# Optimization experiments

Hardware: AMD Instinct MI355X
Metric: run time of the kernel (lower is better)

Reference implementation:

```python
import jax, jax.numpy as jnp
import numpy as np

D_MODEL = 1024
N_HEADS = 16
HEAD_DIM = D_MODEL // N_HEADS
B, L, E = 2, 2048, 256


def _linear_params(key, d_out, d_in):
    kw, kb = jax.random.split(key)
    lim = 1.0 / np.sqrt(d_in)
    W = jax.random.uniform(kw, (d_out, d_in), jnp.float32, -lim, lim)
    b = jax.random.uniform(kb, (d_out,), jnp.float32, -lim, lim)
    return W, b


def setup_inputs() -> dict:
    key = jax.random.key(0)
    ks = jax.random.split(key, 10)
    x = jax.random.normal(ks[0], (B, L, D_MODEL), jnp.float32)
    kg_embeds = jax.random.normal(ks[1], (B, E, D_MODEL), jnp.float32)
    Wq, bq = _linear_params(ks[2], D_MODEL, D_MODEL)
    Wk, bk = _linear_params(ks[3], D_MODEL, D_MODEL)
    Wv, bv = _linear_params(ks[4], D_MODEL, D_MODEL)
    Wo, bo = _linear_params(ks[5], D_MODEL, D_MODEL)
    Wkk, bkk = _linear_params(ks[6], D_MODEL, D_MODEL)
    Wkv, bkv = _linear_params(ks[7], D_MODEL, D_MODEL)
    Wg, bg = _linear_params(ks[8], D_MODEL, 2 * D_MODEL)
    return {"x": x, "kg_embeds": kg_embeds,
            "Wq": Wq, "bq": bq, "Wk": Wk, "bk": bk, "Wv": Wv, "bv": bv,
            "Wkk": Wkk, "bkk": bkk, "Wkv": Wkv, "bkv": bkv,
            "Wo": Wo, "bo": bo, "Wg": Wg, "bg": bg}


def _heads(t):
    # [B, S, D] -> [B, H, S, hd]
    Bb, S, _ = t.shape
    return t.reshape(Bb, S, N_HEADS, HEAD_DIM).transpose(0, 2, 1, 3)


def reference(x, kg_embeds, Wq, bq, Wk, bk, Wv, bv, Wkk, bkk, Wkv, bkv, Wo, bo, Wg, bg):
    scale = HEAD_DIM ** -0.5
    q = _heads(x @ Wq.T + bq)                      # [B,H,L,hd]
    k = _heads(x @ Wk.T + bk)
    v = _heads(x @ Wv.T + bv)
    k_kg = _heads(kg_embeds @ Wkk.T + bkk)         # [B,H,E,hd]
    v_kg = _heads(kg_embeds @ Wkv.T + bkv)
    k_aug = jnp.concatenate([k, k_kg], axis=2)     # [B,H,L+E,hd]
    v_aug = jnp.concatenate([v, v_kg], axis=2)
    scores = jnp.einsum('bhld,bhmd->bhlm', q, k_aug) * scale  # [B,H,L,L+E]
    attn = jax.nn.softmax(scores, axis=-1)
    out = jnp.einsum('bhlm,bhmd->bhld', attn, v_aug)           # [B,H,L,hd]
    out = out.transpose(0, 2, 1, 3).reshape(x.shape)            # [B,L,D]
    kg_global = jnp.broadcast_to(kg_embeds.mean(axis=1, keepdims=True), x.shape)
    gate = jax.nn.sigmoid(jnp.concatenate([out, kg_global], axis=-1) @ Wg.T + bg)
    return gate * (out @ Wo.T + bo) + (1.0 - gate) * x
```

## Files before the change

### kernel.cpp

```cpp
#include <hip/hip_runtime.h>
#include <stdint.h>

typedef unsigned short ushort_t;
typedef __attribute__((ext_vector_type(8))) short short8;
typedef __attribute__((ext_vector_type(4))) short short4v;
typedef __attribute__((ext_vector_type(4))) float f32x4;
typedef __attribute__((ext_vector_type(4))) unsigned uintx4;

#define DEV static __device__ __forceinline__

DEV unsigned short f2bf(float f) {
  unsigned u = __builtin_bit_cast(unsigned, f);
  u += 0x7fffu + ((u >> 16) & 1u);
  return (unsigned short)(u >> 16);
}
DEV float bf2f(unsigned short b) {
  return __builtin_bit_cast(float, (unsigned)b << 16);
}

DEV void gl16(const void* g, void* l) {
  __builtin_amdgcn_global_load_lds(
      (__attribute__((address_space(1))) char*)(unsigned long long)g,
      (__attribute__((address_space(3))) char*)(unsigned)(unsigned long long)l,
      16, 0, 0);
}

DEV f32x4 mfma_bf16(short8 a, short8 b, f32x4 c) {
  return __builtin_amdgcn_mfma_f32_16x16x32_bf16(a, b, c, 0, 0, 0);
}

DEV unsigned cvtpk(float lo, float hi) {
  unsigned r;
  asm("v_cvt_pk_bf16_f32 %0, %1, %2" : "=v"(r) : "v"(lo), "v"(hi));
  return r;
}
DEV void swap_net(unsigned& a, unsigned& b) {
  asm("v_permlane32_swap_b32 %0, %1" : "+v"(a), "+v"(b));
  asm("v_permlane16_swap_b32 %0, %1" : "+v"(a), "+v"(b));
}
DEV float redmax4(float x) {
  unsigned a = __builtin_bit_cast(unsigned, x), b = a;
  asm("v_permlane16_swap_b32 %0, %1" : "+v"(a), "+v"(b));
  float y = fmaxf(__builtin_bit_cast(float, a), __builtin_bit_cast(float, b));
  unsigned c = __builtin_bit_cast(unsigned, y), d = c;
  asm("v_permlane32_swap_b32 %0, %1" : "+v"(c), "+v"(d));
  return fmaxf(__builtin_bit_cast(float, c), __builtin_bit_cast(float, d));
}
DEV float lanebcast(float v, int srclane) {
  return __builtin_bit_cast(float,
      __builtin_amdgcn_ds_bpermute(srclane * 4, __builtin_bit_cast(int, v)));
}

__global__ __launch_bounds__(256) void k_cvt_all(
    const float* __restrict__ x, const float* __restrict__ kg,
    const float* __restrict__ Wq, const float* __restrict__ Wk, const float* __restrict__ Wv,
    const float* __restrict__ Wkk, const float* __restrict__ Wkv,
    const float* __restrict__ Wo, const float* __restrict__ Wg,
    ushort_t* __restrict__ xh, ushort_t* __restrict__ kgh,
    ushort_t* __restrict__ WB1, ushort_t* __restrict__ WB2, ushort_t* __restrict__ WB3) {
  const int b = blockIdx.x;
  if (b >= 10752) {
    const int i = (b - 10752) * 256 + threadIdx.x;
    const int r = i >> 8, c = (i & 255) * 4;
    const float4 v = *(const float4*)(Wg + (size_t)r * 2048 + c);
    short4v o;
    o.x = (short)f2bf(v.x); o.y = (short)f2bf(v.y); o.z = (short)f2bf(v.z); o.w = (short)f2bf(v.w);
    *(short4v*)(WB3 + 1048576 + (size_t)r * 1024 + c) = o;
    return;
  }
  const float* src;
  ushort_t* dst;
  int off;
  if (b < 4096)       { src = x;   dst = xh;            off = b; }
  else if (b < 4608)  { src = kg;  dst = kgh;           off = b - 4096; }
  else if (b < 5632)  { src = Wq;  dst = WB1;           off = b - 4608; }
  else if (b < 6656)  { src = Wk;  dst = WB1 + 1048576; off = b - 5632; }
  else if (b < 7680)  { src = Wv;  dst = WB1 + 2097152; off = b - 6656; }
  else if (b < 8704)  { src = Wkk; dst = WB2;           off = b - 7680; }
  else if (b < 9728)  { src = Wkv; dst = WB2 + 1048576; off = b - 8704; }
  else                { src = Wo;  dst = WB3;           off = b - 9728; }
  const int i = off * 1024 + threadIdx.x * 4;
  const float4 v = *(const float4*)(src + i);
  short4v o;
  o.x = (short)f2bf(v.x); o.y = (short)f2bf(v.y); o.z = (short)f2bf(v.z); o.w = (short)f2bf(v.w);
  *(short4v*)(dst + i) = o;
}

__global__ __launch_bounds__(256) void k_kgmean(const float* __restrict__ kg, float* __restrict__ out) {
  const int i = blockIdx.x * 256 + threadIdx.x;
  const int b = i >> 10, d = i & 1023;
  float s = 0.f;
  #pragma unroll 4
  for (int e = 0; e < 256; e++) s += kg[((size_t)b * 256 + e) * 1024 + d];
  out[i] = s * (1.0f / 256.0f);
}

__global__ __launch_bounds__(256) void k_g2(const float* __restrict__ kgm, const float* __restrict__ Wg,
                                            const float* __restrict__ bg, float* __restrict__ g2) {
  const int w = threadIdx.x >> 6, l = threadIdx.x & 63;
  const int idx = blockIdx.x * 4 + w;
  const int b = idx >> 10, n = idx & 1023;
  const float* wr = Wg + (size_t)n * 2048 + 1024;
  const float* mb = kgm + b * 1024;
  float s = 0.f;
  #pragma unroll
  for (int j = 0; j < 16; j++) s += mb[j * 64 + l] * wr[j * 64 + l];
  #pragma unroll
  for (int m = 32; m >= 1; m >>= 1) s += __shfl_xor(s, m);
  if (l == 0) g2[idx] = s + bg[n];
}

__global__ __launch_bounds__(256, 3) void k_mm128(
    const ushort_t* __restrict__ A0, const ushort_t* __restrict__ B0,
    const ushort_t* __restrict__ A1, const ushort_t* __restrict__ B1,
    const float* __restrict__ f0, const float* __restrict__ f1, const float* __restrict__ f2,
    const float* __restrict__ f3, const float* __restrict__ f4,
    ushort_t* __restrict__ o0, ushort_t* __restrict__ o1, ushort_t* __restrict__ o2) {
  __shared__ __align__(16) char SHb[49152];
  const int tid = threadIdx.x;
  const int w = tid >> 6, l = tid & 63;
  const int wr = w >> 1, wc = w & 1;
  const int fr = l & 15, fg = l >> 4;

  int m0, n0, iskg = 0;
  {
    const int wg = ((int)blockIdx.x & 7) * 104 + ((int)blockIdx.x >> 3);
    if (wg < 768) { m0 = (wg / 24) * 128; n0 = (wg % 24) * 128; }
    else          { const int k = wg - 768; iskg = 1; m0 = (k >> 4) * 128; n0 = (k & 15) * 128; }
  }
  const ushort_t* A = iskg ? A1 : A0;
  const ushort_t* B = iskg ? B1 : B0;

  int grow[2], gcb[2];
  #pragma unroll
  for (int j = 0; j < 2; j++) {
    const int beta = j * 256 + tid;
    const int rp = beta >> 3;
    const int u = (beta & 7) ^ (rp & 7);
    grow[j] = 2 * rp + (u >> 2);
    gcb[j] = u & 3;
  }
  const char* gA[2];
  const char* gB[2];
  #pragma unroll
  for (int j = 0; j < 2; j++) {
    gA[j] = (const char*)A + (size_t)(m0 + grow[j]) * 2048 + gcb[j] * 16;
    gB[j] = (const char*)B + (size_t)(n0 + grow[j]) * 2048 + gcb[j] * 16;
  }

  auto stage = [&](int s, int kt) {
    char* As = SHb + s * 16384;
    char* Bs = As + 8192;
    const int ko = kt * 64;
    #pragma unroll
    for (int j = 0; j < 2; j++) {
      gl16(gA[j] + ko, As + j * 4096 + tid * 16);
      gl16(gB[j] + ko, Bs + j * 4096 + tid * 16);
    }
  };

  int aoff[4], boff[4];
  #pragma unroll
  for (int i = 0; i < 4; i++) {
    const int rowa = wr * 64 + i * 16 + fr;
    aoff[i] = (rowa >> 1) * 128 + ((((rowa & 1) << 6) | (fg << 4)) ^ (((rowa >> 1) & 7) << 4));
    const int rowb = wc * 64 + i * 16 + fr;
    boff[i] = (rowb >> 1) * 128 + ((((rowb & 1) << 6) | (fg << 4)) ^ (((rowb >> 1) & 7) << 4));
  }

  f32x4 acc[4][4] = {};

  stage(0, 0);
  stage(1, 1);
  int sc = 0, sn2 = 2;
  for (int kt = 0; kt < 32; kt++) {
    if (kt < 31) asm volatile("s_waitcnt vmcnt(4)" ::: "memory");
    else         asm volatile("s_waitcnt vmcnt(0)" ::: "memory");
    __builtin_amdgcn_s_barrier();
    asm volatile("" ::: "memory");
    if (kt < 30) stage(sn2, kt + 2);
    const char* Ab = SHb + sc * 16384;
    const char* Bb = Ab + 8192;
    short8 af[4], bf[4];
    #pragma unroll
    for (int j = 0; j < 4; j++) bf[j] = *(const short8*)(Bb + boff[j]);
    #pragma unroll
    for (int i = 0; i < 4; i++) af[i] = *(const short8*)(Ab + aoff[i]);
    __builtin_amdgcn_s_setprio(1);
    #pragma unroll
    for (int i = 0; i < 4; i++)
      #pragma unroll
      for (int j = 0; j < 4; j++)
        acc[i][j] = mfma_bf16(af[i], bf[j], acc[i][j]);
    __builtin_amdgcn_s_setprio(0);
    sc++; if (sc == 3) sc = 0;
    sn2++; if (sn2 == 3) sn2 = 0;
  }
  __syncthreads();

  const int sec = n0 >> 10;
  const bool isV = (!iskg && sec == 2) || (iskg && sec == 1);

  if (isV) {
    ushort_t* SHs = (ushort_t*)SHb;
    const float* bV = iskg ? f4 : f2;
    const int bidx = iskg ? (m0 >> 8) : (m0 >> 11);
    const int colbase = iskg ? (2048 + (m0 & 255)) : (m0 & 2047);
    #pragma unroll
    for (int i = 0; i < 4; i++) {
      #pragma unroll
      for (int j = 0; j < 4; j++) {
        const int nl = wc * 64 + j * 16 + fr;
        const int ml0 = wr * 64 + i * 16 + fg * 4;
        const float bb = bV[(n0 & 1023) + nl];
        short4v pk;
        #pragma unroll
        for (int r = 0; r < 4; r++) pk[r] = (short)f2bf(acc[i][j][r] + bb);
        *(short4v*)(SHs + nl * 128 + (ml0 ^ ((nl & 7) << 3))) = pk;
      }
    }
    __syncthreads();
    const int row = tid >> 1, half = tid & 1;
    const int h = ((n0 & 1023) >> 6) + (row >> 6);
    const int d = row & 63;
    ushort_t* dst = o2 + ((size_t)(bidx * 16 + h) * 64 + d) * 2304 + colbase + half * 64;
    const ushort_t* srow2 = SHs + row * 128;
    #pragma unroll
    for (int k2 = 0; k2 < 8; k2++) {
      const int me = (half * 64 + k2 * 8) ^ ((row & 7) << 3);
      *(short8*)(dst + k2 * 8) = *(const short8*)(srow2 + me);
    }
    return;
  }

  #pragma unroll
  for (int i = 0; i < 4; i++) {
    #pragma unroll
    for (int j = 0; j < 4; j++) {
      const int nn = (n0 & 1023) + wc * 64 + j * 16 + fr;
      const int h = nn >> 6, d = nn & 63;
      #pragma unroll
      for (int r = 0; r < 4; r++) {
        const int m = m0 + wr * 64 + i * 16 + fg * 4 + r;
        const float v = acc[i][j][r];
        if (iskg) {
          const int b = m >> 8, e = m & 255;
          o1[((size_t)(b * 16 + h) * 2304 + 2048 + e) * 64 + d] = f2bf(v + f3[nn]);
        } else if (sec == 0) {
          const int b = m >> 11, lq = m & 2047;
          o0[((size_t)(b * 16 + h) * 2048 + lq) * 64 + d] = f2bf((v + f0[nn]) * 0.18033688f);
        } else {
          const int b = m >> 11, lq = m & 2047;
          o1[((size_t)(b * 16 + h) * 2304 + lq) * 64 + d] = f2bf(v + f1[nn]);
        }
      }
    }
  }
}

__global__ __launch_bounds__(256, 2) void k_mmout(
    const ushort_t* __restrict__ Og, const ushort_t* __restrict__ WB3,
    const float* __restrict__ bo, const float* __restrict__ g2v,
    const float* __restrict__ x, float* __restrict__ y) {
  __shared__ __align__(16) char SHb[61440];
  const int tid = threadIdx.x;
  const int w = tid >> 6, l = tid & 63;
  const int wr = w >> 1, wc = w & 1;
  const int fr = l & 15, fg = l >> 4;

  const int wg = ((int)blockIdx.x & 7) * 64 + ((int)blockIdx.x >> 3);
  const int m0 = (wg >> 3) * 64, n0 = (wg & 7) * 128;

  const int rpA = tid >> 3, uA = (tid & 7) ^ (rpA & 7);
  const char* gAp = (const char*)Og + (size_t)(m0 + 2 * rpA + (uA >> 2)) * 2048 + (uA & 3) * 16;
  int grow[2], gcb[2];
  #pragma unroll
  for (int j = 0; j < 2; j++) {
    const int beta = j * 256 + tid;
    const int rp = beta >> 3;
    const int u = (beta & 7) ^ (rp & 7);
    grow[j] = 2 * rp + (u >> 2);
    gcb[j] = u & 3;
  }
  const char* gBo[2];
  const char* gBg[2];
  #pragma unroll
  for (int j = 0; j < 2; j++) {
    gBo[j] = (const char*)WB3 + (size_t)(n0 + grow[j]) * 2048 + gcb[j] * 16;
    gBg[j] = (const char*)(WB3 + 1048576) + (size_t)(n0 + grow[j]) * 2048 + gcb[j] * 16;
  }

  auto stage = [&](int s, int kt) {
    char* As = SHb + s * 20480;
    const int ko = kt * 64;
    gl16(gAp + ko, As + tid * 16);
    #pragma unroll
    for (int j = 0; j < 2; j++) {
      gl16(gBo[j] + ko, As + 4096 + j * 4096 + tid * 16);
      gl16(gBg[j] + ko, As + 12288 + j * 4096 + tid * 16);
    }
  };

  int aoff[2], boff[4];
  #pragma unroll
  for (int i = 0; i < 2; i++) {
    const int rowa = wr * 32 + i * 16 + fr;
    aoff[i] = (rowa >> 1) * 128 + ((((rowa & 1) << 6) | (fg << 4)) ^ (((rowa >> 1) & 7) << 4));
  }
  #pragma unroll
  for (int j = 0; j < 4; j++) {
    const int rowb = wc * 64 + j * 16 + fr;
    boff[j] = (rowb >> 1) * 128 + ((((rowb & 1) << 6) | (fg << 4)) ^ (((rowb >> 1) & 7) << 4));
  }

  f32x4 ao[2][4] = {};
  f32x4 ag[2][4] = {};

  stage(0, 0);
  stage(1, 1);
  int sc = 0, sn2 = 2;
  for (int kt = 0; kt < 32; kt++) {
    if (kt < 31) asm volatile("s_waitcnt vmcnt(5)" ::: "memory");
    else         asm volatile("s_waitcnt vmcnt(0)" ::: "memory");
    __builtin_amdgcn_s_barrier();
    asm volatile("" ::: "memory");
    if (kt < 30) stage(sn2, kt + 2);
    const char* Ab = SHb + sc * 20480;
    short8 af[2], bof[4], bgf[4];
    #pragma unroll
    for (int i = 0; i < 2; i++) af[i] = *(const short8*)(Ab + aoff[i]);
    #pragma unroll
    for (int j = 0; j < 4; j++) {
      bof[j] = *(const short8*)(Ab + 4096 + boff[j]);
      bgf[j] = *(const short8*)(Ab + 12288 + boff[j]);
    }
    __builtin_amdgcn_s_setprio(1);
    #pragma unroll
    for (int i = 0; i < 2; i++)
      #pragma unroll
      for (int j = 0; j < 4; j++) {
        ao[i][j] = mfma_bf16(af[i], bof[j], ao[i][j]);
        ag[i][j] = mfma_bf16(af[i], bgf[j], ag[i][j]);
      }
    __builtin_amdgcn_s_setprio(0);
    sc++; if (sc == 3) sc = 0;
    sn2++; if (sn2 == 3) sn2 = 0;
  }

  const int bidx = m0 >> 11;
  #pragma unroll
  for (int i = 0; i < 2; i++) {
    #pragma unroll
    for (int j = 0; j < 4; j++) {
      const int nn = n0 + wc * 64 + j * 16 + fr;
      const float bb = bo[nn];
      const float gg = g2v[bidx * 1024 + nn];
      #pragma unroll
      for (int r = 0; r < 4; r++) {
        const int m = m0 + wr * 32 + i * 16 + fg * 4 + r;
        const float co = ao[i][j][r] + bb;
        const float cg = ag[i][j][r] + gg;
        const float gate = 1.0f / (1.0f + __builtin_amdgcn_exp2f(cg * -1.4426950408889634f));
        const float xv = x[(size_t)m * 1024 + nn];
        y[(size_t)m * 1024 + nn] = xv + gate * (co - xv);
      }
    }
  }
}

__global__ __launch_bounds__(256, 4) void k_attn(
    const ushort_t* __restrict__ Qg, const ushort_t* __restrict__ Kg,
    const ushort_t* __restrict__ Vtg, ushort_t* __restrict__ Og) {
  __shared__ __align__(16) ushort_t Ks[2][64 * 64];
  __shared__ __align__(16) ushort_t Vs[2][64 * 64];
  const int tid = threadIdx.x;
  const int w = tid >> 6, l = tid & 63;
  const int fr = l & 15, fg = l >> 4;

  const int id = blockIdx.y * gridDim.x + blockIdx.x;
  const int bh = (id & 7) * 4 + ((id >> 3) >> 5);
  const int q0 = ((id >> 3) & 31) * 64 + w * 16;

  short8 qf[2];
  {
    const short* qrow = (const short*)(Qg + ((size_t)bh * 2048 + q0 + fr) * 64);
    qf[0] = *(const short8*)(qrow + fg * 8);
    qf[1] = *(const short8*)(qrow + 32 + fg * 8);
  }

  constexpr short ONE = 0x3F80;
  const short8 ones = {ONE, ONE, ONE, ONE, ONE, ONE, ONE, ONE};

  f32x4 o[4] = {};
  f32x4 lacc = {};
  float mrun = -1.0e30f;

  const int rsub = tid >> 3;
  const int cS = ((tid & 7) * 16) ^ ((rsub & 7) << 4);
  const char* kbase = (const char*)(Kg + (size_t)bh * 2304 * 64);
  const char* vbase = (const char*)(Vtg + (size_t)bh * 64 * 2304);

  auto stage = [&](int nb, int tile) {
    #pragma unroll
    for (int j = 0; j < 2; j++) {
      const int row = j * 32 + rsub;
      gl16(kbase + (size_t)(tile * 64 + row) * 128 + cS,
           (char*)&Ks[nb][0] + j * 4096 + tid * 16);
      gl16(vbase + (size_t)row * 4608 + tile * 128 + cS,
           (char*)&Vs[nb][0] + j * 4096 + tid * 16);
    }
  };

  stage(0, 0);

  const int rswz = (fr & 7) << 4;

  for (int mt = 0; mt < 36; mt++) {
    __syncthreads();
    if (mt < 35) stage((mt + 1) & 1, mt + 1);

    const char* Kb = (const char*)&Ks[mt & 1][0];
    const char* Vb = (const char*)&Vs[mt & 1][0];

    f32x4 s[4];
    #pragma unroll
    for (int t = 0; t < 4; t++) {
      const int rb = (t * 16 + fr) * 128 + fg * 16;
      const short8 k0 = *(const short8*)(Kb + (rb ^ rswz));
      const short8 k1 = *(const short8*)(Kb + ((rb + 64) ^ rswz));
      f32x4 z = {};
      z = mfma_bf16(k0, qf[0], z);
      z = mfma_bf16(k1, qf[1], z);
      s[t] = z;
    }

    float m = fmaxf(s[0][0], s[0][1]);
    m = fmaxf(fmaxf(m, s[0][2]), s[0][3]);
    m = fmaxf(fmaxf(m, s[1][0]), s[1][1]);
    m = fmaxf(fmaxf(m, s[1][2]), s[1][3]);
    m = fmaxf(fmaxf(m, s[2][0]), s[2][1]);
    m = fmaxf(fmaxf(m, s[2][2]), s[2][3]);
    m = fmaxf(fmaxf(m, s[3][0]), s[3][1]);
    m = fmaxf(fmaxf(m, s[3][2]), s[3][3]);
    const float mx = redmax4(m);
    if (__any(mx - mrun > 11.5416f)) {
      const float mn = fmaxf(mrun, mx);
      const float al = __builtin_amdgcn_exp2f(mrun - mn);
      mrun = mn;
      float ab[4];
      #pragma unroll
      for (int r = 0; r < 4; r++) ab[r] = lanebcast(al, fg * 4 + r);
      #pragma unroll
      for (int r = 0; r < 4; r++) {
        lacc[r] *= ab[r];
        #pragma unroll
        for (int dt = 0; dt < 4; dt++) o[dt][r] *= ab[r];
      }
    }
    #pragma unroll
    for (int t = 0; t < 4; t++)
      #pragma unroll
      for (int r = 0; r < 4; r++)
        s[t][r] = __builtin_amdgcn_exp2f(s[t][r] - mrun);

    #pragma unroll
    for (int c = 0; c < 2; c++) {
      unsigned a0 = cvtpk(s[2 * c][0], s[2 * c][1]);
      unsigned b0 = cvtpk(s[2 * c + 1][0], s[2 * c + 1][1]);
      unsigned a1 = cvtpk(s[2 * c][2], s[2 * c][3]);
      unsigned b1 = cvtpk(s[2 * c + 1][2], s[2 * c + 1][3]);
      swap_net(a0, b0);
      swap_net(a1, b1);
      uintx4 u;
      u.x = a0; u.y = a1; u.z = b0; u.w = b1;
      const short8 pf = __builtin_bit_cast(short8, u);
      lacc = mfma_bf16(pf, ones, lacc);
      #pragma unroll
      for (int dt = 0; dt < 4; dt++) {
        const int vb2 = ((dt * 16 + fr) * 128) + fg * 16 + c * 64;
        const short8 vf = *(const short8*)(Vb + (vb2 ^ rswz));
        o[dt] = mfma_bf16(pf, vf, o[dt]);
      }
    }
  }

  const int b = bh >> 4, h = bh & 15;
  #pragma unroll
  for (int r = 0; r < 4; r++) {
    const float inv = 1.0f / lacc[r];
    const int q = q0 + fg * 4 + r;
    ushort_t* orow = Og + ((size_t)b * 2048 + q) * 1024 + h * 64;
    #pragma unroll
    for (int dt = 0; dt < 4; dt++) orow[dt * 16 + fr] = f2bf(o[dt][r] * inv);
  }
}

extern "C" void kernel_launch(void* const* d_in, const int* in_sizes, int n_in,
                              void* d_out, int out_size, void* d_ws, size_t ws_size,
                              hipStream_t stream) {
  (void)in_sizes; (void)n_in; (void)out_size; (void)ws_size;
  const float* x   = (const float*)d_in[0];
  const float* kg  = (const float*)d_in[1];
  const float* Wq  = (const float*)d_in[2];
  const float* bq  = (const float*)d_in[3];
  const float* Wk  = (const float*)d_in[4];
  const float* bk  = (const float*)d_in[5];
  const float* Wv  = (const float*)d_in[6];
  const float* bv  = (const float*)d_in[7];
  const float* Wkk = (const float*)d_in[8];
  const float* bkk = (const float*)d_in[9];
  const float* Wkv = (const float*)d_in[10];
  const float* bkv = (const float*)d_in[11];
  const float* Wo  = (const float*)d_in[12];
  const float* bo  = (const float*)d_in[13];
  const float* Wg  = (const float*)d_in[14];
  const float* bg  = (const float*)d_in[15];
  float* y = (float*)d_out;

  char* ws = (char*)d_ws;
  size_t off = 0;
  auto take = [&](size_t bytes) {
    char* p = ws + off;
    off += (bytes + 255) & ~(size_t)255;
    return p;
  };
  ushort_t* xh   = (ushort_t*)take((size_t)4096 * 1024 * 2);
  ushort_t* kgh  = (ushort_t*)take((size_t)512 * 1024 * 2);
  ushort_t* WB1  = (ushort_t*)take((size_t)3072 * 1024 * 2);
  ushort_t* WB2  = (ushort_t*)take((size_t)2048 * 1024 * 2);
  ushort_t* WB3  = (ushort_t*)take((size_t)2048 * 1024 * 2);
  ushort_t* Qg   = (ushort_t*)take((size_t)32 * 2048 * 64 * 2);
  ushort_t* Kaug = (ushort_t*)take((size_t)32 * 2304 * 64 * 2);
  ushort_t* Vt   = (ushort_t*)take((size_t)32 * 2304 * 64 * 2);
  ushort_t* Og   = (ushort_t*)take((size_t)4096 * 1024 * 2);
  float* kgm     = (float*)take(2048 * 4);
  float* g2      = (float*)take(2048 * 4);

  k_cvt_all<<<11776, 256, 0, stream>>>(x, kg, Wq, Wk, Wv, Wkk, Wkv, Wo, Wg,
                                       xh, kgh, WB1, WB2, WB3);
  k_kgmean<<<8, 256, 0, stream>>>(kg, kgm);
  k_g2<<<512, 256, 0, stream>>>(kgm, Wg, bg, g2);

  k_mm128<<<832, 256, 0, stream>>>(xh, WB1, kgh, WB2,
                                   bq, bk, bv, bkk, bkv, Qg, Kaug, Vt);
  k_attn<<<dim3(32, 32), 256, 0, stream>>>(Qg, Kaug, Vt, Og);
  k_mmout<<<512, 256, 0, stream>>>(Og, WB3, bo, g2, x, y);
}
```

Measured before the change: 177.1 us.

## Fold kg-mean into convert kernel, remap QKV GEMM tiles, simplify attention staging addresses

The separate kg-mean kernel becomes 8 extra blocks of the conversion kernel, which removes one launch. The QKV projection GEMM remaps workgroup-to-tile assignment into 8x3 tile groups so that concurrently running blocks share A and B rows in L2. The attention K/V staging precomputes base pointers per thread to reduce address arithmetic in the inner loop. The mean blocks are scheduled last and each loops 256 times, so they may add a tail to the conversion kernel.

```diff
diff --git a/kernel.cpp b/kernel.cpp
--- a/kernel.cpp
+++ b/kernel.cpp
@@ -57,8 +57,18 @@
     const float* __restrict__ Wkk, const float* __restrict__ Wkv,
     const float* __restrict__ Wo, const float* __restrict__ Wg,
     ushort_t* __restrict__ xh, ushort_t* __restrict__ kgh,
-    ushort_t* __restrict__ WB1, ushort_t* __restrict__ WB2, ushort_t* __restrict__ WB3) {
+    ushort_t* __restrict__ WB1, ushort_t* __restrict__ WB2, ushort_t* __restrict__ WB3,
+    float* __restrict__ kgm) {
   const int b = blockIdx.x;
+  if (b >= 11776) {
+    const int i = (b - 11776) * 256 + threadIdx.x;
+    const int bb = i >> 10, d = i & 1023;
+    float s = 0.f;
+    #pragma unroll 4
+    for (int e = 0; e < 256; e++) s += kg[((size_t)bb * 256 + e) * 1024 + d];
+    kgm[i] = s * (1.0f / 256.0f);
+    return;
+  }
   if (b >= 10752) {
     const int i = (b - 10752) * 256 + threadIdx.x;
     const int r = i >> 8, c = (i & 255) * 4;
@@ -86,15 +96,6 @@
   *(short4v*)(dst + i) = o;
 }
 
-__global__ __launch_bounds__(256) void k_kgmean(const float* __restrict__ kg, float* __restrict__ out) {
-  const int i = blockIdx.x * 256 + threadIdx.x;
-  const int b = i >> 10, d = i & 1023;
-  float s = 0.f;
-  #pragma unroll 4
-  for (int e = 0; e < 256; e++) s += kg[((size_t)b * 256 + e) * 1024 + d];
-  out[i] = s * (1.0f / 256.0f);
-}
-
 __global__ __launch_bounds__(256) void k_g2(const float* __restrict__ kgm, const float* __restrict__ Wg,
                                             const float* __restrict__ bg, float* __restrict__ g2) {
   const int w = threadIdx.x >> 6, l = threadIdx.x & 63;
@@ -125,8 +126,13 @@
   int m0, n0, iskg = 0;
   {
     const int wg = ((int)blockIdx.x & 7) * 104 + ((int)blockIdx.x >> 3);
-    if (wg < 768) { m0 = (wg / 24) * 128; n0 = (wg % 24) * 128; }
-    else          { const int k = wg - 768; iskg = 1; m0 = (k >> 4) * 128; n0 = (k & 15) * 128; }
+    if (wg < 768) {
+      const int c = wg / 24, r = wg % 24;
+      m0 = ((c & 3) * 8 + (r & 7)) * 128;
+      n0 = ((c >> 2) * 3 + (r >> 3)) * 128;
+    } else {
+      const int k = wg - 768; iskg = 1; m0 = (k >> 4) * 128; n0 = (k & 15) * 128;
+    }
   }
   const ushort_t* A = iskg ? A1 : A0;
   const ushort_t* B = iskg ? B1 : B0;
@@ -397,17 +403,16 @@
 
   const int rsub = tid >> 3;
   const int cS = ((tid & 7) * 16) ^ ((rsub & 7) << 4);
-  const char* kbase = (const char*)(Kg + (size_t)bh * 2304 * 64);
-  const char* vbase = (const char*)(Vtg + (size_t)bh * 64 * 2304);
+  const char* kb0 = (const char*)(Kg + (size_t)bh * 2304 * 64) + (size_t)rsub * 128 + cS;
+  const char* vb0 = (const char*)(Vtg + (size_t)bh * 64 * 2304) + (size_t)rsub * 4608 + cS;
+  char* kd0 = (char*)&Ks[0][0] + tid * 16;
+  char* vd0 = (char*)&Vs[0][0] + tid * 16;
 
   auto stage = [&](int nb, int tile) {
     #pragma unroll
     for (int j = 0; j < 2; j++) {
-      const int row = j * 32 + rsub;
-      gl16(kbase + (size_t)(tile * 64 + row) * 128 + cS,
-           (char*)&Ks[nb][0] + j * 4096 + tid * 16);
-      gl16(vbase + (size_t)row * 4608 + tile * 128 + cS,
-           (char*)&Vs[nb][0] + j * 4096 + tid * 16);
+      gl16(kb0 + (size_t)tile * 8192 + j * 4096, kd0 + nb * 8192 + j * 4096);
+      gl16(vb0 + j * 147456 + tile * 128,        vd0 + nb * 8192 + j * 4096);
     }
   };
 
@@ -536,9 +541,8 @@
   float* kgm     = (float*)take(2048 * 4);
   float* g2      = (float*)take(2048 * 4);
 
-  k_cvt_all<<<11776, 256, 0, stream>>>(x, kg, Wq, Wk, Wv, Wkk, Wkv, Wo, Wg,
-                                       xh, kgh, WB1, WB2, WB3);
-  k_kgmean<<<8, 256, 0, stream>>>(kg, kgm);
+  k_cvt_all<<<11784, 256, 0, stream>>>(x, kg, Wq, Wk, Wv, Wkk, Wkv, Wo, Wg,
+                                       xh, kgh, WB1, WB2, WB3, kgm);
   k_g2<<<512, 256, 0, stream>>>(kgm, Wg, bg, g2);
 
   k_mm128<<<832, 256, 0, stream>>>(xh, WB1, kgh, WB2,
```

Result: no change. 177.9 us (+0.5%).
